# Performance work log

Hardware: AMD Instinct MI355X
Metric: run time of the kernel (lower is better)

## Reference

```python
import jax, jax.numpy as jnp
import numpy as np

N = 4096      # nodes
D = 256       # in_dim == out_dim (residual forces equality)
H = 4         # n_heads
E = 131072    # edges (avg degree 32)
LN_EPS = 1e-5


def setup_inputs() -> dict:
    key = jax.random.key(0)
    ks = jax.random.split(key, 6)
    s = 1.0 / np.sqrt(D)
    node_features = jax.random.normal(ks[0], (N, D), dtype=jnp.float32)
    edge_index = jax.random.randint(ks[1], (2, E), 0, N, dtype=jnp.int64)
    in_proj_w = (jax.random.normal(ks[2], (3 * D, D), dtype=jnp.float32) * s)
    in_proj_b = jnp.zeros((3 * D,), jnp.float32)
    out_proj_w = (jax.random.normal(ks[3], (D, D), dtype=jnp.float32) * s)
    out_proj_b = jnp.zeros((D,), jnp.float32)
    proj_w = (jax.random.normal(ks[4], (D, D), dtype=jnp.float32) * s)
    proj_b = jnp.zeros((D,), jnp.float32)
    ln_gamma = jnp.ones((D,), jnp.float32)
    ln_beta = jnp.zeros((D,), jnp.float32)
    return {
        "node_features": node_features, "edge_index": edge_index,
        "in_proj_w": in_proj_w, "in_proj_b": in_proj_b,
        "out_proj_w": out_proj_w, "out_proj_b": out_proj_b,
        "proj_w": proj_w, "proj_b": proj_b,
        "ln_gamma": ln_gamma, "ln_beta": ln_beta,
    }


def _allowed_mask(edge_index, n):
    # True where attention is allowed (edges symmetrized + self loops)
    src, dst = edge_index[0], edge_index[1]
    m = jnp.zeros((n, n), dtype=bool)
    m = m.at[src, dst].set(True)
    m = m.at[dst, src].set(True)
    diag = jnp.arange(n)
    return m.at[diag, diag].set(True)


def reference(node_features, edge_index, in_proj_w, in_proj_b,
              out_proj_w, out_proj_b, proj_w, proj_b, ln_gamma, ln_beta):
    n, d = node_features.shape
    hd = d // H
    allowed = _allowed_mask(edge_index, n)

    # packed QKV projection (torch MultiheadAttention in_proj)
    qkv = node_features @ in_proj_w.T + in_proj_b          # [N, 3D]
    q, k, v = jnp.split(qkv, 3, axis=-1)
    q = q.reshape(n, H, hd).transpose(1, 0, 2)             # [H, N, hd]
    k = k.reshape(n, H, hd).transpose(1, 0, 2)
    v = v.reshape(n, H, hd).transpose(1, 0, 2)

    scores = jnp.einsum('hqd,hkd->hqk', q, k) / np.sqrt(hd)  # [H, N, N]
    scores = jnp.where(allowed[None], scores, -jnp.inf)
    attn = jax.nn.softmax(scores, axis=-1)
    ctx = jnp.einsum('hqk,hkd->hqd', attn, v)               # [H, N, hd]
    ctx = ctx.transpose(1, 0, 2).reshape(n, d)              # [N, D]
    attended = ctx @ out_proj_w.T + out_proj_b

    out = attended @ proj_w.T + proj_b                      # proj (dropout=eval identity)
    y = out + node_features                                 # residual
    mu = jnp.mean(y, axis=-1, keepdims=True)
    var = jnp.var(y, axis=-1, keepdims=True)
    return (y - mu) / jnp.sqrt(var + LN_EPS) * ln_gamma + ln_beta
```

## Files before the change

kernel.cpp:

```cpp
#include <hip/hip_runtime.h>
#include <math.h>

#define N_NODES 4096
#define DIM 256
#define HEADS 4
#define HDIM 64
#define NEDGE 131072
#define MAXNBR 256
#define MASK_WORDS 128

typedef __attribute__((ext_vector_type(8))) short short8;
typedef __attribute__((ext_vector_type(4))) float float4v;

__device__ inline unsigned short f2b(float f) {
    unsigned u = __float_as_uint(f);
    unsigned r = u + 0x7fffu + ((u >> 16) & 1u);
    return (unsigned short)(r >> 16);
}
__device__ inline float b2f(unsigned short s) { return __uint_as_float(((unsigned)s) << 16); }
__device__ inline float bl(unsigned u) { return __uint_as_float(u << 16); }
__device__ inline float bh(unsigned u) { return __uint_as_float(u & 0xffff0000u); }

__global__ __launch_bounds__(256)
void prep_kernel(const float* __restrict__ x, const float* __restrict__ w_in,
                 const float* __restrict__ wp, const float* __restrict__ wout,
                 const float* __restrict__ bout, const float* __restrict__ bp,
                 unsigned short* __restrict__ x_bf, unsigned short* __restrict__ w_in_bf,
                 unsigned short* __restrict__ wc, float* __restrict__ bc) {
    const int b = blockIdx.x;
    const int tid = threadIdx.x;
    if (b < 1024) {
        int t = b * 1024 + tid * 4;
        float4 v = *(const float4*)&x[t];
        ushort4 o;
        o.x = f2b(v.x); o.y = f2b(v.y); o.z = f2b(v.z); o.w = f2b(v.w);
        *(ushort4*)&x_bf[t] = o;
    } else if (b < 1024 + 192) {
        int t = (b - 1024) * 1024 + tid * 4;
        float4 v = *(const float4*)&w_in[t];
        ushort4 o;
        o.x = f2b(v.x); o.y = f2b(v.y); o.z = f2b(v.z); o.w = f2b(v.w);
        *(ushort4*)&w_in_bf[t] = o;
    } else {
        int bb = b - 1216;
        int i = (bb >> 4) * 16 + (tid >> 4);
        int j = (bb & 15) * 16 + (tid & 15);
        float a0 = 0.f, a1 = 0.f, a2 = 0.f, a3 = 0.f;
        for (int k = 0; k < 256; k += 4) {
            a0 = fmaf(wp[i * 256 + k + 0], wout[(k + 0) * 256 + j], a0);
            a1 = fmaf(wp[i * 256 + k + 1], wout[(k + 1) * 256 + j], a1);
            a2 = fmaf(wp[i * 256 + k + 2], wout[(k + 2) * 256 + j], a2);
            a3 = fmaf(wp[i * 256 + k + 3], wout[(k + 3) * 256 + j], a3);
        }
        wc[i * 256 + j] = f2b((a0 + a1) + (a2 + a3));
        if (bb == 0) {
            float b0 = bp[tid], b1 = 0.f, b2 = 0.f, b3 = 0.f;
            for (int k = 0; k < 256; k += 4) {
                b0 = fmaf(wp[tid * 256 + k + 0], bout[k + 0], b0);
                b1 = fmaf(wp[tid * 256 + k + 1], bout[k + 1], b1);
                b2 = fmaf(wp[tid * 256 + k + 2], bout[k + 2], b2);
                b3 = fmaf(wp[tid * 256 + k + 3], bout[k + 3], b3);
            }
            bc[tid] = (b0 + b1) + (b2 + b3);
        }
    }
}

__global__ void build_mask_kernel(const int* __restrict__ eidx, unsigned int* __restrict__ mask) {
    int t = blockIdx.x * blockDim.x + threadIdx.x;
    if (t < NEDGE) {
        int s = eidx[t];
        int d = eidx[NEDGE + t];
        atomicOr(&mask[s * MASK_WORDS + (d >> 5)], 1u << (d & 31));
        atomicOr(&mask[d * MASK_WORDS + (s >> 5)], 1u << (s & 31));
    }
}

__global__ __launch_bounds__(256)
void extract_csr_kernel(const unsigned int* __restrict__ mask,
                        int* __restrict__ nnz, int* __restrict__ cols) {
    const int wave = threadIdx.x >> 6;
    const int lane = threadIdx.x & 63;
    const int i = blockIdx.x * 4 + wave;
    const unsigned int* row = mask + (size_t)i * MASK_WORDS;
    unsigned w0 = row[lane * 2];
    unsigned w1 = row[lane * 2 + 1];
    int wi = i >> 5;
    if (wi == lane * 2)     w0 |= 1u << (i & 31);
    if (wi == lane * 2 + 1) w1 |= 1u << (i & 31);
    int cnt = __popc(w0) + __popc(w1);
    int incl = cnt;
#pragma unroll
    for (int off = 1; off < 64; off <<= 1) {
        int v = __shfl_up(incl, off, 64);
        if (lane >= off) incl += v;
    }
    int c = incl - cnt;
    int total = __shfl(incl, 63, 64);
    while (w0) {
        int b = __ffs(w0) - 1;
        if (c < MAXNBR) cols[(size_t)i * MAXNBR + c] = lane * 64 + b;
        ++c; w0 &= w0 - 1u;
    }
    while (w1) {
        int b = __ffs(w1) - 1;
        if (c < MAXNBR) cols[(size_t)i * MAXNBR + c] = lane * 64 + 32 + b;
        ++c; w1 &= w1 - 1u;
    }
    if (lane == 0) nnz[i] = total > MAXNBR ? MAXNBR : total;
}

template <bool OUT_BF16>
__global__ __launch_bounds__(256)
void mfma_gemm64(const unsigned short* __restrict__ A, const unsigned short* __restrict__ B,
                 const float* __restrict__ bias, const float* __restrict__ resid,
                 void* __restrict__ Cout, int M, int Nc, int K) {
    __shared__ unsigned short As[64 * 64];
    __shared__ unsigned short Bs[64 * 64];
    const int tid  = threadIdx.x;
    const int lane = tid & 63;
    const int wave = tid >> 6;
    const int brow = blockIdx.y * 64;
    const int bcol = blockIdx.x * 64;

    float4v acc[4];
#pragma unroll
    for (int t = 0; t < 4; ++t) acc[t] = (float4v){0.f, 0.f, 0.f, 0.f};

    const int quad = lane >> 4;
    const int l16  = lane & 15;

    for (int k0 = 0; k0 < K; k0 += 64) {
        __syncthreads();
#pragma unroll
        for (int it = 0; it < 2; ++it) {
            int c = it * 256 + tid;
            int row = c >> 3;
            int col = c & 7;
            int sw  = col ^ (row & 7);
            uint4 va = *(const uint4*)&A[(size_t)(brow + row) * K + k0 + col * 8];
            uint4 vb = *(const uint4*)&B[(size_t)(bcol + row) * K + k0 + col * 8];
            *(uint4*)&As[row * 64 + sw * 8] = va;
            *(uint4*)&Bs[row * 64 + sw * 8] = vb;
        }
        __syncthreads();
#pragma unroll
        for (int kk = 0; kk < 2; ++kk) {
            short8 af, bf[4];
            {
                int row = wave * 16 + l16;
                int sw = (kk * 4 + quad) ^ (row & 7);
                af = *(const short8*)&As[row * 64 + sw * 8];
            }
#pragma unroll
            for (int nt = 0; nt < 4; ++nt) {
                int row = nt * 16 + l16;
                int sw = (kk * 4 + quad) ^ (row & 7);
                bf[nt] = *(const short8*)&Bs[row * 64 + sw * 8];
            }
#pragma unroll
            for (int nt = 0; nt < 4; ++nt)
                acc[nt] = __builtin_amdgcn_mfma_f32_16x16x32_bf16(af, bf[nt], acc[nt], 0, 0, 0);
        }
    }

#pragma unroll
    for (int nt = 0; nt < 4; ++nt) {
        int colg = bcol + nt * 16 + l16;
        float bsv = bias[colg];
#pragma unroll
        for (int reg = 0; reg < 4; ++reg) {
            int rowg = brow + wave * 16 + quad * 4 + reg;
            float v = acc[nt][reg] + bsv;
            if (resid) v += resid[(size_t)rowg * Nc + colg];
            if (OUT_BF16)
                ((unsigned short*)Cout)[(size_t)rowg * Nc + colg] = f2b(v);
            else
                ((float*)Cout)[(size_t)rowg * Nc + colg] = v;
        }
    }
}

__global__ __launch_bounds__(256)
void attn_sparse_kernel(const unsigned short* __restrict__ qkv, const int* __restrict__ cols,
                        const int* __restrict__ nnz, unsigned short* __restrict__ ctx) {
    __shared__ int cols_s[MAXNBR];

    const int wave = threadIdx.x >> 6;
    const int lane = threadIdx.x & 63;
    const int ng = lane >> 3;
    const int dg = lane & 7;
    const int i = blockIdx.x;
    const int h = wave;

    cols_s[threadIdx.x] = cols[(size_t)i * MAXNBR + threadIdx.x];
    int count = nnz[i];
    if (count > MAXNBR) count = MAXNBR;

    float qf[8];
    {
        uint4 qv = *(const uint4*)&qkv[(size_t)i * 768 + h * HDIM + dg * 8];
        qf[0] = bl(qv.x); qf[1] = bh(qv.x);
        qf[2] = bl(qv.y); qf[3] = bh(qv.y);
        qf[4] = bl(qv.z); qf[5] = bh(qv.z);
        qf[6] = bl(qv.w); qf[7] = bh(qv.w);
    }
    __syncthreads();

    const unsigned short* kB = qkv + DIM + h * HDIM + dg * 8;
    const unsigned short* vB = qkv + 2 * DIM + h * HDIM + dg * 8;
    float a0 = 0.f, a1 = 0.f, a2 = 0.f, a3 = 0.f, a4 = 0.f, a5 = 0.f, a6 = 0.f, a7 = 0.f;
    float esum = 0.f;

    for (int t0 = 0; t0 < count; t0 += 8) {
        int t = t0 + ng;
        int j = cols_s[min(t, count - 1)];
        uint4 kv = *(const uint4*)&kB[(size_t)j * 768];
        uint4 vv = *(const uint4*)&vB[(size_t)j * 768];
        float s = qf[0] * bl(kv.x) + qf[1] * bh(kv.x)
                + qf[2] * bl(kv.y) + qf[3] * bh(kv.y)
                + qf[4] * bl(kv.z) + qf[5] * bh(kv.z)
                + qf[6] * bl(kv.w) + qf[7] * bh(kv.w);
        s += __shfl_xor(s, 1, 64);
        s += __shfl_xor(s, 2, 64);
        s += __shfl_xor(s, 4, 64);
        float e = (t < count) ? expf(s * 0.125f) : 0.f;
        esum += e;
        a0 = fmaf(e, bl(vv.x), a0); a1 = fmaf(e, bh(vv.x), a1);
        a2 = fmaf(e, bl(vv.y), a2); a3 = fmaf(e, bh(vv.y), a3);
        a4 = fmaf(e, bl(vv.z), a4); a5 = fmaf(e, bh(vv.z), a5);
        a6 = fmaf(e, bl(vv.w), a6); a7 = fmaf(e, bh(vv.w), a7);
    }
#pragma unroll
    for (int off = 8; off <= 32; off <<= 1) {
        esum += __shfl_xor(esum, off, 64);
        a0 += __shfl_xor(a0, off, 64); a1 += __shfl_xor(a1, off, 64);
        a2 += __shfl_xor(a2, off, 64); a3 += __shfl_xor(a3, off, 64);
        a4 += __shfl_xor(a4, off, 64); a5 += __shfl_xor(a5, off, 64);
        a6 += __shfl_xor(a6, off, 64); a7 += __shfl_xor(a7, off, 64);
    }
    if (ng == 0) {
        float inv = 1.0f / esum;
        uint4 w;
        w.x = (unsigned)f2b(a0 * inv) | ((unsigned)f2b(a1 * inv) << 16);
        w.y = (unsigned)f2b(a2 * inv) | ((unsigned)f2b(a3 * inv) << 16);
        w.z = (unsigned)f2b(a4 * inv) | ((unsigned)f2b(a5 * inv) << 16);
        w.w = (unsigned)f2b(a6 * inv) | ((unsigned)f2b(a7 * inv) << 16);
        *(uint4*)&ctx[(size_t)i * DIM + h * HDIM + dg * 8] = w;
    }
}

__global__ __launch_bounds__(256)
void ln_kernel(const float* __restrict__ y, const float* __restrict__ gamma,
               const float* __restrict__ beta, float* __restrict__ out) {
    const int wave = threadIdx.x >> 6;
    const int lane = threadIdx.x & 63;
    const int i = blockIdx.x * 4 + wave;
    float4 v = ((const float4*)(y + (size_t)i * DIM))[lane];
    float s = v.x + v.y + v.z + v.w;
    float ss = v.x * v.x + v.y * v.y + v.z * v.z + v.w * v.w;
#pragma unroll
    for (int off = 32; off > 0; off >>= 1) {
        s += __shfl_xor(s, off, 64);
        ss += __shfl_xor(ss, off, 64);
    }
    float mean = s * (1.f / 256.f);
    float var = ss * (1.f / 256.f) - mean * mean;
    float rstd = rsqrtf(var + 1e-5f);
    float4 g = ((const float4*)gamma)[lane];
    float4 b = ((const float4*)beta)[lane];
    float4 o;
    o.x = (v.x - mean) * rstd * g.x + b.x;
    o.y = (v.y - mean) * rstd * g.y + b.y;
    o.z = (v.z - mean) * rstd * g.z + b.z;
    o.w = (v.w - mean) * rstd * g.w + b.w;
    ((float4*)(out + (size_t)i * DIM))[lane] = o;
}

extern "C" void kernel_launch(void* const* d_in, const int* in_sizes, int n_in,
                              void* d_out, int out_size, void* d_ws, size_t ws_size,
                              hipStream_t stream) {
    const float* x      = (const float*)d_in[0];
    const int*   eidx   = (const int*)d_in[1];
    const float* w_in   = (const float*)d_in[2];
    const float* b_in   = (const float*)d_in[3];
    const float* w_out  = (const float*)d_in[4];
    const float* b_out  = (const float*)d_in[5];
    const float* w_p    = (const float*)d_in[6];
    const float* b_p    = (const float*)d_in[7];
    const float* gamma  = (const float*)d_in[8];
    const float* beta   = (const float*)d_in[9];
    float* out = (float*)d_out;

    char* ws = (char*)d_ws;
    unsigned int*   mask    = (unsigned int*)(ws + 0);
    int*            nnz     = (int*)(ws + 2097152);
    int*            cols    = (int*)(ws + 2113536);
    unsigned short* qkv_bf  = (unsigned short*)(ws + 6307840);
    unsigned short* ctx_bf  = (unsigned short*)(ws + 12599296);
    float*          ybuf    = (float*)(ws + 14696448);
    unsigned short* x_bf    = (unsigned short*)(ws + 18890752);
    unsigned short* w_in_bf = (unsigned short*)(ws + 20987904);
    unsigned short* wc_bf   = (unsigned short*)(ws + 21381120);
    float*          bc      = (float*)(ws + 21512192);

    prep_kernel<<<1472, 256, 0, stream>>>(x, w_in, w_p, w_out, b_out, b_p,
                                          x_bf, w_in_bf, wc_bf, bc);
    hipMemsetAsync(mask, 0, N_NODES * MASK_WORDS * 4, stream);
    build_mask_kernel<<<(NEDGE + 255) / 256, 256, 0, stream>>>(eidx, mask);
    extract_csr_kernel<<<N_NODES / 4, 256, 0, stream>>>(mask, nnz, cols);
    {
        dim3 grid(768 / 64, N_NODES / 64);
        mfma_gemm64<true><<<grid, 256, 0, stream>>>(x_bf, w_in_bf, b_in, nullptr,
                                                    qkv_bf, N_NODES, 768, DIM);
    }
    attn_sparse_kernel<<<N_NODES, 256, 0, stream>>>(qkv_bf, cols, nnz, ctx_bf);
    {
        dim3 grid(DIM / 64, N_NODES / 64);
        mfma_gemm64<false><<<grid, 256, 0, stream>>>(ctx_bf, wc_bf, bc, x,
                                                     ybuf, N_NODES, DIM, DIM);
    }
    ln_kernel<<<N_NODES / 4, 256, 0, stream>>>(ybuf, gamma, beta, out);
}
```

Before: 143.7 us.

## Fuse CSR extraction into sparse attention and unroll neighbor loop by two

Removes the separate extract_csr kernel: each attention block now loads its row of the adjacency bitmask into shared memory and builds the neighbor column list with a wave-0 prefix scan before the attention loop. This drops one launch and the global write and read of the cols/nnz arrays. The gather loop also handles two groups of eight neighbors per iteration to raise memory-level parallelism. The trade-off is that three waves sit idle during the scan, and the extra registers could lower occupancy.

```diff
diff --git a/kernel.cpp b/kernel.cpp
--- a/kernel.cpp
+++ b/kernel.cpp
@@ -76,40 +76,6 @@
     }
 }
 
-__global__ __launch_bounds__(256)
-void extract_csr_kernel(const unsigned int* __restrict__ mask,
-                        int* __restrict__ nnz, int* __restrict__ cols) {
-    const int wave = threadIdx.x >> 6;
-    const int lane = threadIdx.x & 63;
-    const int i = blockIdx.x * 4 + wave;
-    const unsigned int* row = mask + (size_t)i * MASK_WORDS;
-    unsigned w0 = row[lane * 2];
-    unsigned w1 = row[lane * 2 + 1];
-    int wi = i >> 5;
-    if (wi == lane * 2)     w0 |= 1u << (i & 31);
-    if (wi == lane * 2 + 1) w1 |= 1u << (i & 31);
-    int cnt = __popc(w0) + __popc(w1);
-    int incl = cnt;
-#pragma unroll
-    for (int off = 1; off < 64; off <<= 1) {
-        int v = __shfl_up(incl, off, 64);
-        if (lane >= off) incl += v;
-    }
-    int c = incl - cnt;
-    int total = __shfl(incl, 63, 64);
-    while (w0) {
-        int b = __ffs(w0) - 1;
-        if (c < MAXNBR) cols[(size_t)i * MAXNBR + c] = lane * 64 + b;
-        ++c; w0 &= w0 - 1u;
-    }
-    while (w1) {
-        int b = __ffs(w1) - 1;
-        if (c < MAXNBR) cols[(size_t)i * MAXNBR + c] = lane * 64 + 32 + b;
-        ++c; w1 &= w1 - 1u;
-    }
-    if (lane == 0) nnz[i] = total > MAXNBR ? MAXNBR : total;
-}
-
 template <bool OUT_BF16>
 __global__ __launch_bounds__(256)
 void mfma_gemm64(const unsigned short* __restrict__ A, const unsigned short* __restrict__ B,
@@ -182,20 +148,22 @@
 }
 
 __global__ __launch_bounds__(256)
-void attn_sparse_kernel(const unsigned short* __restrict__ qkv, const int* __restrict__ cols,
-                        const int* __restrict__ nnz, unsigned short* __restrict__ ctx) {
+void attn_sparse_kernel(const unsigned short* __restrict__ qkv,
+                        const unsigned int* __restrict__ mask,
+                        unsigned short* __restrict__ ctx) {
+    __shared__ unsigned int rowmask[MASK_WORDS];
     __shared__ int cols_s[MAXNBR];
-
-    const int wave = threadIdx.x >> 6;
-    const int lane = threadIdx.x & 63;
+    __shared__ int count_s;
+
+    const int tid  = threadIdx.x;
+    const int wave = tid >> 6;
+    const int lane = tid & 63;
     const int ng = lane >> 3;
     const int dg = lane & 7;
     const int i = blockIdx.x;
     const int h = wave;
 
-    cols_s[threadIdx.x] = cols[(size_t)i * MAXNBR + threadIdx.x];
-    int count = nnz[i];
-    if (count > MAXNBR) count = MAXNBR;
+    if (tid < MASK_WORDS) rowmask[tid] = mask[(size_t)i * MASK_WORDS + tid];
 
     float qf[8];
     {
@@ -207,29 +175,72 @@
     }
     __syncthreads();
 
+    if (wave == 0) {
+        unsigned w0 = rowmask[lane * 2];
+        unsigned w1 = rowmask[lane * 2 + 1];
+        int wi = i >> 5;
+        if (wi == lane * 2)     w0 |= 1u << (i & 31);
+        if (wi == lane * 2 + 1) w1 |= 1u << (i & 31);
+        int cnt = __popc(w0) + __popc(w1);
+        int incl = cnt;
+#pragma unroll
+        for (int off = 1; off < 64; off <<= 1) {
+            int v = __shfl_up(incl, off, 64);
+            if (lane >= off) incl += v;
+        }
+        int c = incl - cnt;
+        int total = __shfl(incl, 63, 64);
+        while (w0) {
+            int b = __ffs(w0) - 1;
+            if (c < MAXNBR) cols_s[c] = lane * 64 + b;
+            ++c; w0 &= w0 - 1u;
+        }
+        while (w1) {
+            int b = __ffs(w1) - 1;
+            if (c < MAXNBR) cols_s[c] = lane * 64 + 32 + b;
+            ++c; w1 &= w1 - 1u;
+        }
+        if (lane == 0) count_s = total > MAXNBR ? MAXNBR : total;
+    }
+    __syncthreads();
+    const int count = count_s;
+
     const unsigned short* kB = qkv + DIM + h * HDIM + dg * 8;
     const unsigned short* vB = qkv + 2 * DIM + h * HDIM + dg * 8;
     float a0 = 0.f, a1 = 0.f, a2 = 0.f, a3 = 0.f, a4 = 0.f, a5 = 0.f, a6 = 0.f, a7 = 0.f;
     float esum = 0.f;
 
-    for (int t0 = 0; t0 < count; t0 += 8) {
-        int t = t0 + ng;
-        int j = cols_s[min(t, count - 1)];
-        uint4 kv = *(const uint4*)&kB[(size_t)j * 768];
-        uint4 vv = *(const uint4*)&vB[(size_t)j * 768];
-        float s = qf[0] * bl(kv.x) + qf[1] * bh(kv.x)
-                + qf[2] * bl(kv.y) + qf[3] * bh(kv.y)
-                + qf[4] * bl(kv.z) + qf[5] * bh(kv.z)
-                + qf[6] * bl(kv.w) + qf[7] * bh(kv.w);
-        s += __shfl_xor(s, 1, 64);
-        s += __shfl_xor(s, 2, 64);
-        s += __shfl_xor(s, 4, 64);
-        float e = (t < count) ? expf(s * 0.125f) : 0.f;
-        esum += e;
-        a0 = fmaf(e, bl(vv.x), a0); a1 = fmaf(e, bh(vv.x), a1);
-        a2 = fmaf(e, bl(vv.y), a2); a3 = fmaf(e, bh(vv.y), a3);
-        a4 = fmaf(e, bl(vv.z), a4); a5 = fmaf(e, bh(vv.z), a5);
-        a6 = fmaf(e, bl(vv.w), a6); a7 = fmaf(e, bh(vv.w), a7);
+    for (int t0 = 0; t0 < count; t0 += 16) {
+        int tA = t0 + ng;
+        int tB = t0 + 8 + ng;
+        int jA = cols_s[min(tA, count - 1)];
+        int jB = cols_s[min(tB, count - 1)];
+        uint4 kvA = *(const uint4*)&kB[(size_t)jA * 768];
+        uint4 vvA = *(const uint4*)&vB[(size_t)jA * 768];
+        uint4 kvB = *(const uint4*)&kB[(size_t)jB * 768];
+        uint4 vvB = *(const uint4*)&vB[(size_t)jB * 768];
+        float sA = qf[0] * bl(kvA.x) + qf[1] * bh(kvA.x)
+                 + qf[2] * bl(kvA.y) + qf[3] * bh(kvA.y)
+                 + qf[4] * bl(kvA.z) + qf[5] * bh(kvA.z)
+                 + qf[6] * bl(kvA.w) + qf[7] * bh(kvA.w);
+        float sB = qf[0] * bl(kvB.x) + qf[1] * bh(kvB.x)
+                 + qf[2] * bl(kvB.y) + qf[3] * bh(kvB.y)
+                 + qf[4] * bl(kvB.z) + qf[5] * bh(kvB.z)
+                 + qf[6] * bl(kvB.w) + qf[7] * bh(kvB.w);
+        sA += __shfl_xor(sA, 1, 64);  sB += __shfl_xor(sB, 1, 64);
+        sA += __shfl_xor(sA, 2, 64);  sB += __shfl_xor(sB, 2, 64);
+        sA += __shfl_xor(sA, 4, 64);  sB += __shfl_xor(sB, 4, 64);
+        float eA = (tA < count) ? expf(sA * 0.125f) : 0.f;
+        float eB = (tB < count) ? expf(sB * 0.125f) : 0.f;
+        esum += eA + eB;
+        a0 = fmaf(eA, bl(vvA.x), a0); a1 = fmaf(eA, bh(vvA.x), a1);
+        a2 = fmaf(eA, bl(vvA.y), a2); a3 = fmaf(eA, bh(vvA.y), a3);
+        a4 = fmaf(eA, bl(vvA.z), a4); a5 = fmaf(eA, bh(vvA.z), a5);
+        a6 = fmaf(eA, bl(vvA.w), a6); a7 = fmaf(eA, bh(vvA.w), a7);
+        a0 = fmaf(eB, bl(vvB.x), a0); a1 = fmaf(eB, bh(vvB.x), a1);
+        a2 = fmaf(eB, bl(vvB.y), a2); a3 = fmaf(eB, bh(vvB.y), a3);
+        a4 = fmaf(eB, bl(vvB.z), a4); a5 = fmaf(eB, bh(vvB.z), a5);
+        a6 = fmaf(eB, bl(vvB.w), a6); a7 = fmaf(eB, bh(vvB.w), a7);
     }
 #pragma unroll
     for (int off = 8; off <= 32; off <<= 1) {
@@ -294,27 +305,24 @@
 
     char* ws = (char*)d_ws;
     unsigned int*   mask    = (unsigned int*)(ws + 0);
-    int*            nnz     = (int*)(ws + 2097152);
-    int*            cols    = (int*)(ws + 2113536);
-    unsigned short* qkv_bf  = (unsigned short*)(ws + 6307840);
-    unsigned short* ctx_bf  = (unsigned short*)(ws + 12599296);
-    float*          ybuf    = (float*)(ws + 14696448);
-    unsigned short* x_bf    = (unsigned short*)(ws + 18890752);
-    unsigned short* w_in_bf = (unsigned short*)(ws + 20987904);
-    unsigned short* wc_bf   = (unsigned short*)(ws + 21381120);
-    float*          bc      = (float*)(ws + 21512192);
+    unsigned short* qkv_bf  = (unsigned short*)(ws + 2097152);
+    unsigned short* ctx_bf  = (unsigned short*)(ws + 8388608);
+    float*          ybuf    = (float*)(ws + 10485760);
+    unsigned short* x_bf    = (unsigned short*)(ws + 14680064);
+    unsigned short* w_in_bf = (unsigned short*)(ws + 16777216);
+    unsigned short* wc_bf   = (unsigned short*)(ws + 17170432);
+    float*          bc      = (float*)(ws + 17301504);
 
     prep_kernel<<<1472, 256, 0, stream>>>(x, w_in, w_p, w_out, b_out, b_p,
                                           x_bf, w_in_bf, wc_bf, bc);
     hipMemsetAsync(mask, 0, N_NODES * MASK_WORDS * 4, stream);
     build_mask_kernel<<<(NEDGE + 255) / 256, 256, 0, stream>>>(eidx, mask);
-    extract_csr_kernel<<<N_NODES / 4, 256, 0, stream>>>(mask, nnz, cols);
     {
         dim3 grid(768 / 64, N_NODES / 64);
         mfma_gemm64<true><<<grid, 256, 0, stream>>>(x_bf, w_in_bf, b_in, nullptr,
                                                     qkv_bf, N_NODES, 768, DIM);
     }
-    attn_sparse_kernel<<<N_NODES, 256, 0, stream>>>(qkv_bf, cols, nnz, ctx_bf);
+    attn_sparse_kernel<<<N_NODES, 256, 0, stream>>>(qkv_bf, mask, ctx_bf);
     {
         dim3 grid(DIM / 64, N_NODES / 64);
         mfma_gemm64<false><<<grid, 256, 0, stream>>>(ctx_bf, wc_bf, bc, x,
```

New measurement: 141.7 us. No clear change (-1.4%).
